# Performance work log

Measured on AMD Instinct MI355X. Metric: run time of the kernel, lower is better.

Reference implementation:

```python
import jax, jax.numpy as jnp
import numpy as np

SEQ_LEN = 1
INPUT = 2048
HIDDEN = 2048
CLASSES = 10
K = int(np.floor(np.sqrt(HIDDEN)))            # avgKernelSize = 45
NUM_EH = (HIDDEN - K) // K + 1                # 45 pooled features
LENGTHS = (32, 128, 512)                      # EHlengths (window sizes)
EST_DIM = NUM_EH * len(LENGTHS) * 2           # mean + variance per (feature, window)
B = 8192


def setup_inputs() -> dict:
    key = jax.random.key(0)
    ks = jax.random.split(key, 7)
    s = 1.0 / np.sqrt(HIDDEN)
    u = lambda k, shape: jax.random.uniform(k, shape, jnp.float32, -s, s)
    return {
        "x": jax.random.normal(ks[0], (B, SEQ_LEN, INPUT), jnp.float32),
        "W_ih": u(ks[1], (HIDDEN, INPUT)),
        "W_hh": u(ks[2], (HIDDEN, HIDDEN)),
        "b_ih": u(ks[3], (HIDDEN,)),
        "b_hh": u(ks[4], (HIDDEN,)),
        "W_lin": u(ks[5], (CLASSES, HIDDEN + EST_DIM)),
        "b_lin": u(ks[6], (CLASSES,)),
    }


def _sliding_stats(pooled):
    """Causal sliding-window mean/variance over the batch/stream axis.

    pooled: (B, F). Returns (B, F, J, 2) with [..., 0]=mean, [..., 1]=var.
    This is the exact quantity the VarEH exponential histograms approximate
    (streaming mean/variance over the last L elements added).
    """
    n = pooled.shape[0]
    cs = jnp.cumsum(pooled, axis=0)
    cs2 = jnp.cumsum(pooled * pooled, axis=0)
    idx = jnp.arange(n)
    outs = []
    for L in LENGTHS:  # small fixed set of window lengths
        zpad = jnp.zeros((L,) + pooled.shape[1:], pooled.dtype)
        cs_l = jnp.concatenate([zpad, cs], axis=0)[:n]
        cs2_l = jnp.concatenate([zpad, cs2], axis=0)[:n]
        cnt = jnp.minimum(idx + 1, L).astype(pooled.dtype)[:, None]
        m = (cs - cs_l) / cnt
        v = (cs2 - cs2_l) / cnt - m * m
        outs.append(jnp.stack([m, v], axis=-1))  # (B, F, 2)
    return jnp.stack(outs, axis=2)  # (B, F, J, 2)


def reference(x, W_ih, W_hh, b_ih, b_hh, W_lin, b_lin):
    b = x.shape[0]
    # Elman RNN, batch_first, h0 = 0. Precompute input projection for all steps.
    xw = jnp.einsum("bsi,hi->bsh", x, W_ih) + b_ih + b_hh  # (B, S, H)

    def step(h, xt):
        h = jnp.tanh(xt + h @ W_hh.T)
        return h, h

    h0 = jnp.zeros((b, HIDDEN), x.dtype)
    _, hs = jax.lax.scan(step, h0, jnp.swapaxes(xw, 0, 1))  # (S, B, H)
    rnn_out = hs[-1]  # (B, H); with seq_len=1 this equals squeeze(rnn_out)

    # AvgPool1d(kernel=K, stride=K) over hidden dim -> (B, NUM_EH)
    pooled = rnn_out[:, : NUM_EH * K].reshape(b, NUM_EH, K).mean(axis=-1)

    # Streaming mean/var estimates across the batch stream (VarEH semantics)
    est = _sliding_stats(pooled).reshape(b, EST_DIM)

    lin_in = jnp.concatenate([rnn_out, est], axis=1)  # (B, H + EST_DIM)
    logits = lin_in @ W_lin.T + b_lin
    return jax.nn.softmax(logits, axis=1)
```

## Files before the change

kernel.cpp:

```cpp
#include <hip/hip_runtime.h>
#include <hip/hip_bf16.h>
#include <math.h>

typedef short s16x8 __attribute__((ext_vector_type(8)));
typedef float f32x4 __attribute__((ext_vector_type(4)));

__device__ inline unsigned short f2bf(float x) {
    unsigned int u = __float_as_uint(x);
    unsigned int r = (u + 0x7fffu + ((u >> 16) & 1u)) >> 16;
    return (unsigned short)r;
}
__device__ inline float bf2f(unsigned short u) {
    return __uint_as_float(((unsigned int)u) << 16);
}

__device__ inline float fast_tanh(float x) {
    float e = __expf(2.0f * x);
    return 1.0f - 2.0f * __builtin_amdgcn_rcpf(e + 1.0f);
}

__global__ void cvtprep_kernel(const float* __restrict__ x,
                               const float* __restrict__ W_ih,
                               const float* __restrict__ W_lin,
                               unsigned short* __restrict__ xb,
                               unsigned short* __restrict__ wb,
                               unsigned short* __restrict__ wlb) {
    int blk = blockIdx.x;
    int tid = threadIdx.x;
    if (blk < 16384) {
        int i = blk * 256 + tid;
        float4 v = ((const float4*)x)[i];
        ushort4 o; o.x = f2bf(v.x); o.y = f2bf(v.y); o.z = f2bf(v.z); o.w = f2bf(v.w);
        ((ushort4*)xb)[i] = o;
    } else if (blk < 20480) {
        int i = (blk - 16384) * 256 + tid;
        float4 v = ((const float4*)W_ih)[i];
        ushort4 o; o.x = f2bf(v.x); o.y = f2bf(v.y); o.z = f2bf(v.z); o.w = f2bf(v.w);
        ((ushort4*)wb)[i] = o;
    } else {
        int idx = (blk - 20480) * 256 + tid;
        if (idx < 37376) {
            int c = idx / 2336, k = idx - c * 2336;
            float v = (c < 10 && k < 2318) ? W_lin[c * 2318 + k] : 0.f;
            wlb[idx] = f2bf(v);
        }
    }
}


#define MFMA_(a, b, c) __builtin_amdgcn_mfma_f32_16x16x32_bf16(a, b, c, 0, 0, 0)

__device__ inline s16x8 frag_ld(const unsigned short* hbase, int row, int ksub, int quad) {
    int slot = (ksub * 4 + quad) ^ (row & 7);
    return *(const s16x8*)(hbase + row * 64 + slot * 8);
}

__device__ inline void stage_u(const unsigned short* __restrict__ gmat, int half,
                               int rowoff, int kt, unsigned short* lmat, int tid) {
    int r = tid >> 3, s = tid & 7;
    int lr = rowoff + r;
    int ks = (s ^ (lr & 7)) << 3;
    const unsigned short* gp = gmat + (size_t)(half * 128 + lr) * 2048 + kt * 64 + ks;
    __builtin_amdgcn_global_load_lds(
        (const __attribute__((address_space(1))) void*)gp,
        (__attribute__((address_space(3))) void*)(lmat + half * 8192 + lr * 64 + s * 8),
        16, 0, 0);
}

#define LOAD_B(ks)                                                       \
    b0 = frag_ld(Bh, bco +  0 + mrow, (ks), quad);                       \
    b1 = frag_ld(Bh, bco + 16 + mrow, (ks), quad);                       \
    b2 = frag_ld(Bh, bco + 32 + mrow, (ks), quad);                       \
    b3 = frag_ld(Bh, bco + 48 + mrow, (ks), quad);

#define LOAD_A(h, ks)                                                    \
    af0 = frag_ld(Ah, (h) * 64 +  0 + mrow, (ks), quad);                 \
    af1 = frag_ld(Ah, (h) * 64 + 16 + mrow, (ks), quad);                 \
    af2 = frag_ld(Ah, (h) * 64 + 32 + mrow, (ks), quad);                 \
    af3 = frag_ld(Ah, (h) * 64 + 48 + mrow, (ks), quad);

#define MFMA_H(hh)                                                       \
    acc[(hh)*4 + 0][0] = MFMA_(af0, b0, acc[(hh)*4 + 0][0]);             \
    acc[(hh)*4 + 0][1] = MFMA_(af0, b1, acc[(hh)*4 + 0][1]);             \
    acc[(hh)*4 + 0][2] = MFMA_(af0, b2, acc[(hh)*4 + 0][2]);             \
    acc[(hh)*4 + 0][3] = MFMA_(af0, b3, acc[(hh)*4 + 0][3]);             \
    acc[(hh)*4 + 1][0] = MFMA_(af1, b0, acc[(hh)*4 + 1][0]);             \
    acc[(hh)*4 + 1][1] = MFMA_(af1, b1, acc[(hh)*4 + 1][1]);             \
    acc[(hh)*4 + 1][2] = MFMA_(af1, b2, acc[(hh)*4 + 1][2]);             \
    acc[(hh)*4 + 1][3] = MFMA_(af1, b3, acc[(hh)*4 + 1][3]);             \
    acc[(hh)*4 + 2][0] = MFMA_(af2, b0, acc[(hh)*4 + 2][0]);             \
    acc[(hh)*4 + 2][1] = MFMA_(af2, b1, acc[(hh)*4 + 2][1]);             \
    acc[(hh)*4 + 2][2] = MFMA_(af2, b2, acc[(hh)*4 + 2][2]);             \
    acc[(hh)*4 + 2][3] = MFMA_(af2, b3, acc[(hh)*4 + 2][3]);             \
    acc[(hh)*4 + 3][0] = MFMA_(af3, b0, acc[(hh)*4 + 3][0]);             \
    acc[(hh)*4 + 3][1] = MFMA_(af3, b1, acc[(hh)*4 + 3][1]);             \
    acc[(hh)*4 + 3][2] = MFMA_(af3, b2, acc[(hh)*4 + 3][2]);             \
    acc[(hh)*4 + 3][3] = MFMA_(af3, b3, acc[(hh)*4 + 3][3]);

#define PHASE_CORE(hh)                                                   \
    __builtin_amdgcn_s_barrier();                                        \
    asm volatile("s_waitcnt lgkmcnt(0)" ::: "memory");                   \
    __builtin_amdgcn_s_setprio(1);                                       \
    MFMA_H(hh);                                                          \
    __builtin_amdgcn_s_setprio(0);

__global__ __launch_bounds__(512) void gemm_tanh_kernel(
    const unsigned short* __restrict__ A, const unsigned short* __restrict__ Bm,
    const float* __restrict__ b_ih, const float* __restrict__ b_hh,
    unsigned short* __restrict__ Hb)
{
    __shared__ __align__(16) unsigned short lds[2][2][16384];

    const int tid  = threadIdx.x;
    const int lane = tid & 63;
    const int wave = tid >> 6;
    const int wgid = blockIdx.x;
    const int xcd  = wgid & 7;
    const int idx  = wgid >> 3;
    const int rblk = xcd * 4 + (idx & 3);
    const int cblk = idx >> 2;
    const int row0 = rblk * 256;
    const int col0 = cblk * 256;
    const int wm   = wave >> 2;
    const int wn   = wave & 3;
    const int quad = lane >> 4;
    const int mrow = lane & 15;
    const int NT   = 32;

    const unsigned short* Ag = A  + (size_t)row0 * 2048;
    const unsigned short* Bg = Bm + (size_t)col0 * 2048;

    f32x4 acc[8][4];
#pragma unroll
    for (int i = 0; i < 8; ++i)
#pragma unroll
        for (int j = 0; j < 4; ++j) acc[i][j] = f32x4{0.f, 0.f, 0.f, 0.f};

    stage_u(Ag, 0, 0,  0, lds[0][0], tid);  stage_u(Ag, 0, 64, 0, lds[0][0], tid);
    stage_u(Ag, 1, 0,  0, lds[0][0], tid);  stage_u(Ag, 1, 64, 0, lds[0][0], tid);
    stage_u(Bg, 0, 0,  0, lds[0][1], tid);  stage_u(Bg, 0, 64, 0, lds[0][1], tid);
    stage_u(Bg, 1, 0,  0, lds[0][1], tid);  stage_u(Bg, 1, 64, 0, lds[0][1], tid);
    stage_u(Bg, 0, 0,  1, lds[1][1], tid);  stage_u(Bg, 0, 64, 1, lds[1][1], tid);
    stage_u(Ag, 0, 0,  1, lds[1][0], tid);  stage_u(Ag, 1, 0,  1, lds[1][0], tid);
    asm volatile("s_waitcnt vmcnt(4)" ::: "memory");
    __builtin_amdgcn_s_barrier();

    for (int t = 0; t < NT; ++t) {
        const int buf = t & 1;
        unsigned short* LA  = lds[buf][0];
        unsigned short* LB  = lds[buf][1];
        unsigned short* NLA = lds[buf ^ 1][0];
        unsigned short* NLB = lds[buf ^ 1][1];
        const unsigned short* Ah = LA + wm * 8192;
        const unsigned short* Bh = LB + (wn >> 1) * 8192;
        const int bco = (wn & 1) * 64;

        s16x8 b0, b1, b2, b3;
        s16x8 af0, af1, af2, af3;

        LOAD_B(0);
        LOAD_A(0, 0);
        if (t + 1 < NT) {
            stage_u(Ag, 0, 64, t + 1, NLA, tid);
            stage_u(Ag, 1, 64, t + 1, NLA, tid);
            stage_u(Bg, 1, 0,  t + 1, NLB, tid);
            stage_u(Bg, 1, 64, t + 1, NLB, tid);
        }
        asm volatile("s_waitcnt lgkmcnt(4)" ::: "memory");
        PHASE_CORE(0);
        __builtin_amdgcn_s_barrier();

        LOAD_A(1, 0);
        PHASE_CORE(1);
        __builtin_amdgcn_s_barrier();

        LOAD_B(1);
        LOAD_A(0, 1);
        asm volatile("s_waitcnt lgkmcnt(4)" ::: "memory");
        PHASE_CORE(0);
        __builtin_amdgcn_s_barrier();

        LOAD_A(1, 1);
        if (t + 2 < NT) {
            stage_u(Bg, 0, 0,  t + 2, LB, tid);
            stage_u(Bg, 0, 64, t + 2, LB, tid);
            stage_u(Ag, 0, 0,  t + 2, LA, tid);
            stage_u(Ag, 1, 0,  t + 2, LA, tid);
        }
        PHASE_CORE(1);
        if (t + 2 < NT) {
            asm volatile("s_waitcnt vmcnt(4)" ::: "memory");
        } else if (t + 1 < NT) {
            asm volatile("s_waitcnt vmcnt(0)" ::: "memory");
        }
        __builtin_amdgcn_s_barrier();
    }

    float bias[4];
#pragma unroll
    for (int j = 0; j < 4; ++j) {
        int gc = col0 + wn * 64 + j * 16 + mrow;
        bias[j] = b_ih[gc] + b_hh[gc];
    }
#pragma unroll
    for (int i = 0; i < 8; ++i) {
#pragma unroll
        for (int rr = 0; rr < 4; ++rr) {
            int grow = row0 + wm * 128 + i * 16 + quad * 4 + rr;
#pragma unroll
            for (int j = 0; j < 4; ++j) {
                int gc = col0 + wn * 64 + j * 16 + mrow;
                float v = acc[i][j][rr] + bias[j];
                Hb[(size_t)grow * 2048 + gc] = f2bf(fast_tanh(v));
            }
        }
    }
}

__global__ __launch_bounds__(256) void pool_kernel(
    const unsigned short* __restrict__ Hb, float* __restrict__ pooled_t) {
    __shared__ unsigned short hs[8 * 2048];
    __shared__ float outs[45 * 8];
    int b0 = blockIdx.x * 8;
    int tid = threadIdx.x;
    const ushort4* src = (const ushort4*)(Hb + (size_t)b0 * 2048);
    ushort4* dst = (ushort4*)hs;
    for (int i = tid; i < 4096; i += 256) dst[i] = src[i];
    __syncthreads();
    for (int o = tid; o < 360; o += 256) {
        int f = o % 45, r = o / 45;
        const unsigned short* row = hs + r * 2048 + f * 45;
        float s = 0.f;
#pragma unroll
        for (int k = 0; k < 45; ++k) s += bf2f(row[k]);
        outs[f * 8 + r] = s * (1.0f / 45.0f);
    }
    __syncthreads();
    for (int o = tid; o < 360; o += 256) {
        int f = o >> 3, r = o & 7;
        pooled_t[f * 8192 + b0 + r] = outs[o];
    }
}

__global__ __launch_bounds__(256) void scan_kernel(
    const float* __restrict__ pooled_t,
    float* __restrict__ cs_t, float* __restrict__ cs2_t,
    float* __restrict__ sums1, float* __restrict__ sums2) {
    __shared__ float t1[256], t2[256];
    int f  = blockIdx.x >> 3;
    int ch = blockIdx.x & 7;
    int tid = threadIdx.x;
    const float* p = pooled_t + f * 8192 + ch * 1024;
    float4 v = ((const float4*)p)[tid];
    float q1[4], q2[4];
    q1[0] = v.x;          q2[0] = v.x * v.x;
    q1[1] = q1[0] + v.y;  q2[1] = q2[0] + v.y * v.y;
    q1[2] = q1[1] + v.z;  q2[2] = q2[1] + v.z * v.z;
    q1[3] = q1[2] + v.w;  q2[3] = q2[2] + v.w * v.w;
    float s1 = q1[3], s2 = q2[3];
    t1[tid] = s1; t2[tid] = s2;
    __syncthreads();
    for (int d = 1; d < 256; d <<= 1) {
        float a1 = (tid >= d) ? t1[tid - d] : 0.f;
        float a2 = (tid >= d) ? t2[tid - d] : 0.f;
        __syncthreads();
        t1[tid] += a1; t2[tid] += a2;
        __syncthreads();
    }
    float r1 = t1[tid] - s1, r2 = t2[tid] - s2;
    float4 o1, o2;
    o1.x = r1 + q1[0]; o1.y = r1 + q1[1]; o1.z = r1 + q1[2]; o1.w = r1 + q1[3];
    o2.x = r2 + q2[0]; o2.y = r2 + q2[1]; o2.z = r2 + q2[2]; o2.w = r2 + q2[3];
    ((float4*)(cs_t  + f * 8192 + ch * 1024))[tid] = o1;
    ((float4*)(cs2_t + f * 8192 + ch * 1024))[tid] = o2;
    if (tid == 255) {
        sums1[f * 8 + ch] = t1[255];
        sums2[f * 8 + ch] = t2[255];
    }
}

#define ESTRIDE 290
__global__ __launch_bounds__(256) void final_kernel(
    const unsigned short* __restrict__ Hb,
    const float* __restrict__ cs_t, const float* __restrict__ cs2_t,
    const float* __restrict__ sums1, const float* __restrict__ sums2,
    const unsigned short* __restrict__ Wb, const float* __restrict__ b_lin,
    float* __restrict__ out) {
    __shared__ unsigned short Es[16 * ESTRIDE];
    __shared__ float eb1[45 * 8], eb2[45 * 8];
    __shared__ float comb[4][16][17];
    int tid = threadIdx.x;
    int lane = tid & 63;
    int wave = tid >> 6;
    int b0 = blockIdx.x * 16;

    if (tid < 45) {
        float a = 0.f, b = 0.f;
#pragma unroll
        for (int c = 0; c < 8; ++c) {
            eb1[tid * 8 + c] = a; a += sums1[tid * 8 + c];
            eb2[tid * 8 + c] = b; b += sums2[tid * 8 + c];
        }
    }
    __syncthreads();

    for (int i = tid; i < 135 * 16; i += 256) {
        int fj = i >> 4, r = i & 15;
        int f = fj / 3, j = fj - 3 * f;
        int b = b0 + r;
        int L = (j == 0) ? 32 : (j == 1) ? 128 : 512;
        const float* c1 = cs_t + f * 8192;
        const float* c2 = cs2_t + f * 8192;
        float a1 = c1[b] + eb1[f * 8 + (b >> 10)];
        float a2 = c2[b] + eb2[f * 8 + (b >> 10)];
        float p1 = 0.f, p2 = 0.f;
        if (b >= L) {
            int ix = b - L;
            p1 = c1[ix] + eb1[f * 8 + (ix >> 10)];
            p2 = c2[ix] + eb2[f * 8 + (ix >> 10)];
        }
        float cnt = (float)((b + 1 < L) ? (b + 1) : L);
        float m = (a1 - p1) / cnt;
        float v = (a2 - p2) / cnt - m * m;
        int d0 = f * 6 + j * 2;
        Es[r * ESTRIDE + d0]     = f2bf(m);
        Es[r * ESTRIDE + d0 + 1] = f2bf(v);
    }
    for (int i = tid; i < 16 * 18; i += 256) {
        int r = i / 18, d = 270 + i % 18;
        Es[r * ESTRIDE + d] = 0;
    }
    __syncthreads();

    const int kh = wave;
    const int quad = lane >> 4;
    const int mrow = lane & 15;

    f32x4 acc = f32x4{0.f, 0.f, 0.f, 0.f};
    const unsigned short* arow = Hb + (size_t)(b0 + mrow) * 2048 + kh * 512 + quad * 8;
    const unsigned short* brow = Wb + (size_t)mrow * 2336 + kh * 512 + quad * 8;
#pragma unroll 4
    for (int k = 0; k < 512; k += 32) {
        s16x8 a = *(const s16x8*)(arow + k);
        s16x8 b = *(const s16x8*)(brow + k);
        acc = __builtin_amdgcn_mfma_f32_16x16x32_bf16(a, b, acc, 0, 0, 0);
    }
    if (kh == 3) {
        const unsigned short* erow = Es + mrow * ESTRIDE + quad * 8;
        const unsigned short* wrow = Wb + (size_t)mrow * 2336 + 2048 + quad * 8;
#pragma unroll
        for (int k = 0; k < 288; k += 32) {
            s16x8 a = *(const s16x8*)(erow + k);
            s16x8 b = *(const s16x8*)(wrow + k);
            acc = __builtin_amdgcn_mfma_f32_16x16x32_bf16(a, b, acc, 0, 0, 0);
        }
    }

#pragma unroll
    for (int r = 0; r < 4; ++r) comb[kh][quad * 4 + r][mrow] = acc[r];
    __syncthreads();

    {
        int r = tid >> 4, c = tid & 15;
        float v = comb[0][r][c] + comb[1][r][c] + comb[2][r][c] + comb[3][r][c];
        comb[0][r][c] = v;
    }
    __syncthreads();

    if (tid < 16) {
        float lg[10];
        float mx = -1e30f;
#pragma unroll
        for (int c = 0; c < 10; ++c) {
            lg[c] = comb[0][tid][c] + b_lin[c];
            mx = fmaxf(mx, lg[c]);
        }
        float s = 0.f;
#pragma unroll
        for (int c = 0; c < 10; ++c) { lg[c] = expf(lg[c] - mx); s += lg[c]; }
        float inv = 1.0f / s;
#pragma unroll
        for (int c = 0; c < 10; ++c) out[(size_t)(b0 + tid) * 10 + c] = lg[c] * inv;
    }
}

extern "C" void kernel_launch(void* const* d_in, const int* in_sizes, int n_in,
                              void* d_out, int out_size, void* d_ws, size_t ws_size,
                              hipStream_t stream) {
    const float* x     = (const float*)d_in[0];
    const float* W_ih  = (const float*)d_in[1];
    const float* b_ih  = (const float*)d_in[3];
    const float* b_hh  = (const float*)d_in[4];
    const float* W_lin = (const float*)d_in[5];
    const float* b_lin = (const float*)d_in[6];
    float* out = (float*)d_out;

    char* ws = (char*)d_ws;
    unsigned short* xb  = (unsigned short*)(ws);
    unsigned short* wb  = (unsigned short*)(ws + 33554432);
    unsigned short* Hb  = (unsigned short*)(ws + 41943040);
    float* pooled_t     = (float*)(ws + 75497472);
    float* cs_t         = (float*)(ws + 76972032);
    float* cs2_t        = (float*)(ws + 78446592);
    unsigned short* wlb = (unsigned short*)(ws + 79921152);
    float* sums1        = (float*)(ws + 79995904);
    float* sums2        = (float*)(ws + 79997344);

    cvtprep_kernel<<<20626, 256, 0, stream>>>(x, W_ih, W_lin, xb, wb, wlb);
    gemm_tanh_kernel<<<256, 512, 0, stream>>>(xb, wb, b_ih, b_hh, Hb);
    pool_kernel<<<1024, 256, 0, stream>>>(Hb, pooled_t);
    scan_kernel<<<360, 256, 0, stream>>>(pooled_t, cs_t, cs2_t, sums1, sums2);
    final_kernel<<<512, 256, 0, stream>>>(Hb, cs_t, cs2_t, sums1, sums2, wlb, b_lin, out);
}
```

Measured before the change: 217.8 us.

## Fuse pooling and hidden-part linear projection into GEMM epilogue via atomics

The GEMM epilogue now stages the tanh output tile in shared memory instead of writing the full bf16 hidden matrix to global memory. From that tile it computes partial average-pool sums and partial logits against W_lin, accumulating both into zeroed global buffers with atomics. The separate pool kernel goes away, and the final kernel only handles the estimate features. This removes a 32 MB write and later re-reads, at the cost of float atomics (non-deterministic summation order), an extra zeroing pass, and more epilogue work in the GEMM.

New measurement: 226.0 us (median of 3 runs). 3.8% more time.

```diff
diff --git a/kernel.cpp b/kernel.cpp
--- a/kernel.cpp
+++ b/kernel.cpp
@@ -24,7 +24,8 @@
                                const float* __restrict__ W_lin,
                                unsigned short* __restrict__ xb,
                                unsigned short* __restrict__ wb,
-                               unsigned short* __restrict__ wlb) {
+                               unsigned short* __restrict__ wlb,
+                               float* __restrict__ zbase) {
     int blk = blockIdx.x;
     int tid = threadIdx.x;
     if (blk < 16384) {
@@ -37,13 +38,14 @@
         float4 v = ((const float4*)W_ih)[i];
         ushort4 o; o.x = f2bf(v.x); o.y = f2bf(v.y); o.z = f2bf(v.z); o.w = f2bf(v.w);
         ((ushort4*)wb)[i] = o;
+    } else if (blk < 20626) {
+        int idx = (blk - 20480) * 256 + tid;
+        int c = idx / 2336, k = idx - c * 2336;
+        float v = (c < 10 && k < 2318) ? W_lin[c * 2318 + k] : 0.f;
+        wlb[idx] = f2bf(v);
     } else {
-        int idx = (blk - 20480) * 256 + tid;
-        if (idx < 37376) {
-            int c = idx / 2336, k = idx - c * 2336;
-            float v = (c < 10 && k < 2318) ? W_lin[c * 2318 + k] : 0.f;
-            wlb[idx] = f2bf(v);
-        }
+        int i = (blk - 20626) * 256 + tid;
+        ((float4*)zbase)[i] = float4{0.f, 0.f, 0.f, 0.f};
     }
 }
 
@@ -107,7 +109,8 @@
 __global__ __launch_bounds__(512) void gemm_tanh_kernel(
     const unsigned short* __restrict__ A, const unsigned short* __restrict__ Bm,
     const float* __restrict__ b_ih, const float* __restrict__ b_hh,
-    unsigned short* __restrict__ Hb)
+    const unsigned short* __restrict__ Wl,
+    float* __restrict__ pooled_t, float* __restrict__ linp)
 {
     __shared__ __align__(16) unsigned short lds[2][2][16384];
 
@@ -196,6 +199,8 @@
         __builtin_amdgcn_s_barrier();
     }
 
+    __syncthreads();
+    unsigned short* T = &lds[0][0][0];
     float bias[4];
 #pragma unroll
     for (int j = 0; j < 4; ++j) {
@@ -206,39 +211,59 @@
     for (int i = 0; i < 8; ++i) {
 #pragma unroll
         for (int rr = 0; rr < 4; ++rr) {
-            int grow = row0 + wm * 128 + i * 16 + quad * 4 + rr;
+            int lrow = wm * 128 + i * 16 + quad * 4 + rr;
 #pragma unroll
             for (int j = 0; j < 4; ++j) {
-                int gc = col0 + wn * 64 + j * 16 + mrow;
+                int lcol = wn * 64 + j * 16 + mrow;
                 float v = acc[i][j][rr] + bias[j];
-                Hb[(size_t)grow * 2048 + gc] = f2bf(fast_tanh(v));
+                int cb = (lcol >> 3) ^ (lrow & 7);
+                T[lrow * 256 + cb * 8 + (lcol & 7)] = f2bf(fast_tanh(v));
             }
         }
     }
-}
-
-__global__ __launch_bounds__(256) void pool_kernel(
-    const unsigned short* __restrict__ Hb, float* __restrict__ pooled_t) {
-    __shared__ unsigned short hs[8 * 2048];
-    __shared__ float outs[45 * 8];
-    int b0 = blockIdx.x * 8;
-    int tid = threadIdx.x;
-    const ushort4* src = (const ushort4*)(Hb + (size_t)b0 * 2048);
-    ushort4* dst = (ushort4*)hs;
-    for (int i = tid; i < 4096; i += 256) dst[i] = src[i];
-    __syncthreads();
-    for (int o = tid; o < 360; o += 256) {
-        int f = o % 45, r = o / 45;
-        const unsigned short* row = hs + r * 2048 + f * 45;
-        float s = 0.f;
-#pragma unroll
-        for (int k = 0; k < 45; ++k) s += bf2f(row[k]);
-        outs[f * 8 + r] = s * (1.0f / 45.0f);
-    }
-    __syncthreads();
-    for (int o = tid; o < 360; o += 256) {
-        int f = o >> 3, r = o & 7;
-        pooled_t[f * 8192 + b0 + r] = outs[o];
+    __syncthreads();
+
+    int f0 = col0 / 45;
+    for (int o = tid; o < 1792; o += 512) {
+        int lrow = o / 7;
+        int fi = o - lrow * 7;
+        int f = f0 + fi;
+        if (f < 45) {
+            int wsb = f * 45, web = wsb + 45;
+            int s = (wsb > col0) ? wsb : col0;
+            int e = (web < col0 + 256) ? web : (col0 + 256);
+            if (s < e) {
+                float sum = 0.f;
+                for (int c = s - col0; c < e - col0; ++c) {
+                    int cb = (c >> 3) ^ (lrow & 7);
+                    sum += bf2f(T[lrow * 256 + cb * 8 + (c & 7)]);
+                }
+                atomicAdd(&pooled_t[f * 8192 + row0 + lrow], sum);
+            }
+        }
+    }
+
+    f32x4 la = f32x4{0.f, 0.f, 0.f, 0.f};
+    f32x4 lb = f32x4{0.f, 0.f, 0.f, 0.f};
+    const int lr0 = wave * 32 + mrow;
+    const int lr1 = lr0 + 16;
+#pragma unroll
+    for (int ks = 0; ks < 8; ++ks) {
+        int c = ks * 32 + quad * 8;
+        s16x8 bfrag = *(const s16x8*)(Wl + (size_t)mrow * 2336 + col0 + c);
+        int cb0 = (c >> 3) ^ (lr0 & 7);
+        s16x8 a0 = *(const s16x8*)(T + lr0 * 256 + cb0 * 8);
+        la = MFMA_(a0, bfrag, la);
+        int cb1 = (c >> 3) ^ (lr1 & 7);
+        s16x8 a1 = *(const s16x8*)(T + lr1 * 256 + cb1 * 8);
+        lb = MFMA_(a1, bfrag, lb);
+    }
+    if (mrow < 10) {
+#pragma unroll
+        for (int rr = 0; rr < 4; ++rr) {
+            atomicAdd(&linp[(size_t)(row0 + wave * 32 + quad * 4 + rr) * 10 + mrow], la[rr]);
+            atomicAdd(&linp[(size_t)(row0 + wave * 32 + 16 + quad * 4 + rr) * 10 + mrow], lb[rr]);
+        }
     }
 }
 
@@ -250,8 +275,10 @@
     int f  = blockIdx.x >> 3;
     int ch = blockIdx.x & 7;
     int tid = threadIdx.x;
+    const float S = 1.0f / 45.0f;
     const float* p = pooled_t + f * 8192 + ch * 1024;
     float4 v = ((const float4*)p)[tid];
+    v.x *= S; v.y *= S; v.z *= S; v.w *= S;
     float q1[4], q2[4];
     q1[0] = v.x;          q2[0] = v.x * v.x;
     q1[1] = q1[0] + v.y;  q2[1] = q2[0] + v.y * v.y;
@@ -280,19 +307,18 @@
 }
 
 #define ESTRIDE 290
-__global__ __launch_bounds__(256) void final_kernel(
-    const unsigned short* __restrict__ Hb,
+__global__ __launch_bounds__(128) void final_kernel(
     const float* __restrict__ cs_t, const float* __restrict__ cs2_t,
     const float* __restrict__ sums1, const float* __restrict__ sums2,
-    const unsigned short* __restrict__ Wb, const float* __restrict__ b_lin,
-    float* __restrict__ out) {
-    __shared__ unsigned short Es[16 * ESTRIDE];
+    const unsigned short* __restrict__ Wb, const float* __restrict__ linp,
+    const float* __restrict__ b_lin, float* __restrict__ out) {
+    __shared__ unsigned short Es[32 * ESTRIDE];
     __shared__ float eb1[45 * 8], eb2[45 * 8];
-    __shared__ float comb[4][16][17];
+    __shared__ float comb[2][16][17];
     int tid = threadIdx.x;
     int lane = tid & 63;
     int wave = tid >> 6;
-    int b0 = blockIdx.x * 16;
+    int b0 = blockIdx.x * 32;
 
     if (tid < 45) {
         float a = 0.f, b = 0.f;
@@ -304,8 +330,8 @@
     }
     __syncthreads();
 
-    for (int i = tid; i < 135 * 16; i += 256) {
-        int fj = i >> 4, r = i & 15;
+    for (int i = tid; i < 135 * 32; i += 128) {
+        int fj = i >> 5, r = i & 31;
         int f = fj / 3, j = fj - 3 * f;
         int b = b0 + r;
         int L = (j == 0) ? 32 : (j == 1) ? 128 : 512;
@@ -326,53 +352,36 @@
         Es[r * ESTRIDE + d0]     = f2bf(m);
         Es[r * ESTRIDE + d0 + 1] = f2bf(v);
     }
-    for (int i = tid; i < 16 * 18; i += 256) {
+    for (int i = tid; i < 32 * 18; i += 128) {
         int r = i / 18, d = 270 + i % 18;
         Es[r * ESTRIDE + d] = 0;
     }
     __syncthreads();
 
-    const int kh = wave;
     const int quad = lane >> 4;
     const int mrow = lane & 15;
 
     f32x4 acc = f32x4{0.f, 0.f, 0.f, 0.f};
-    const unsigned short* arow = Hb + (size_t)(b0 + mrow) * 2048 + kh * 512 + quad * 8;
-    const unsigned short* brow = Wb + (size_t)mrow * 2336 + kh * 512 + quad * 8;
-#pragma unroll 4
-    for (int k = 0; k < 512; k += 32) {
-        s16x8 a = *(const s16x8*)(arow + k);
-        s16x8 b = *(const s16x8*)(brow + k);
+    const unsigned short* erow = Es + (wave * 16 + mrow) * ESTRIDE + quad * 8;
+    const unsigned short* wrow = Wb + (size_t)mrow * 2336 + 2048 + quad * 8;
+#pragma unroll
+    for (int k = 0; k < 288; k += 32) {
+        s16x8 a = *(const s16x8*)(erow + k);
+        s16x8 b = *(const s16x8*)(wrow + k);
         acc = __builtin_amdgcn_mfma_f32_16x16x32_bf16(a, b, acc, 0, 0, 0);
     }
-    if (kh == 3) {
-        const unsigned short* erow = Es + mrow * ESTRIDE + quad * 8;
-        const unsigned short* wrow = Wb + (size_t)mrow * 2336 + 2048 + quad * 8;
-#pragma unroll
-        for (int k = 0; k < 288; k += 32) {
-            s16x8 a = *(const s16x8*)(erow + k);
-            s16x8 b = *(const s16x8*)(wrow + k);
-            acc = __builtin_amdgcn_mfma_f32_16x16x32_bf16(a, b, acc, 0, 0, 0);
-        }
-    }
-
-#pragma unroll
-    for (int r = 0; r < 4; ++r) comb[kh][quad * 4 + r][mrow] = acc[r];
-    __syncthreads();
-
-    {
-        int r = tid >> 4, c = tid & 15;
-        float v = comb[0][r][c] + comb[1][r][c] + comb[2][r][c] + comb[3][r][c];
-        comb[0][r][c] = v;
-    }
-    __syncthreads();
-
-    if (tid < 16) {
+#pragma unroll
+    for (int r = 0; r < 4; ++r) comb[wave][quad * 4 + r][mrow] = acc[r];
+    __syncthreads();
+
+    if (tid < 32) {
+        int w = tid >> 4, r = tid & 15;
+        int grow = b0 + w * 16 + r;
         float lg[10];
         float mx = -1e30f;
 #pragma unroll
         for (int c = 0; c < 10; ++c) {
-            lg[c] = comb[0][tid][c] + b_lin[c];
+            lg[c] = comb[w][r][c] + linp[(size_t)grow * 10 + c] + b_lin[c];
             mx = fmaxf(mx, lg[c]);
         }
         float s = 0.f;
@@ -380,7 +389,7 @@
         for (int c = 0; c < 10; ++c) { lg[c] = expf(lg[c] - mx); s += lg[c]; }
         float inv = 1.0f / s;
 #pragma unroll
-        for (int c = 0; c < 10; ++c) out[(size_t)(b0 + tid) * 10 + c] = lg[c] * inv;
+        for (int c = 0; c < 10; ++c) out[(size_t)grow * 10 + c] = lg[c] * inv;
     }
 }
 
@@ -398,17 +407,16 @@
     char* ws = (char*)d_ws;
     unsigned short* xb  = (unsigned short*)(ws);
     unsigned short* wb  = (unsigned short*)(ws + 33554432);
-    unsigned short* Hb  = (unsigned short*)(ws + 41943040);
-    float* pooled_t     = (float*)(ws + 75497472);
-    float* cs_t         = (float*)(ws + 76972032);
-    float* cs2_t        = (float*)(ws + 78446592);
-    unsigned short* wlb = (unsigned short*)(ws + 79921152);
-    float* sums1        = (float*)(ws + 79995904);
-    float* sums2        = (float*)(ws + 79997344);
-
-    cvtprep_kernel<<<20626, 256, 0, stream>>>(x, W_ih, W_lin, xb, wb, wlb);
-    gemm_tanh_kernel<<<256, 512, 0, stream>>>(xb, wb, b_ih, b_hh, Hb);
-    pool_kernel<<<1024, 256, 0, stream>>>(Hb, pooled_t);
+    float* pooled_t     = (float*)(ws + 41943040);
+    float* linp         = (float*)(ws + 43417600);
+    float* cs_t         = (float*)(ws + 43745280);
+    float* cs2_t        = (float*)(ws + 45219840);
+    unsigned short* wlb = (unsigned short*)(ws + 46694400);
+    float* sums1        = (float*)(ws + 46769152);
+    float* sums2        = (float*)(ws + 46770592);
+
+    cvtprep_kernel<<<21066, 256, 0, stream>>>(x, W_ih, W_lin, xb, wb, wlb, pooled_t);
+    gemm_tanh_kernel<<<256, 512, 0, stream>>>(xb, wb, b_ih, b_hh, wlb, pooled_t, linp);
     scan_kernel<<<360, 256, 0, stream>>>(pooled_t, cs_t, cs2_t, sums1, sums2);
-    final_kernel<<<512, 256, 0, stream>>>(Hb, cs_t, cs2_t, sums1, sums2, wlb, b_lin, out);
-}
+    final_kernel<<<256, 128, 0, stream>>>(cs_t, cs2_t, sums1, sums2, wlb, linp, b_lin, out);
+}
```
